# Performance work log

Hardware: AMD Instinct MI355X
Metric: run time of the kernel (lower is better)

## Reference

```python
import jax, jax.numpy as jnp
import numpy as np

N, E, F_IN, HID, HEADS, OUT, EDIM = 50000, 800000, 128, 64, 2, 40, 5
NEG_SLOPE = 0.2


def setup_inputs() -> dict:
    key = jax.random.key(0)
    ks = jax.random.split(key, 16)
    x = jax.random.normal(ks[0], (N, F_IN), jnp.float32)
    # build edge_index with src != dst so PyG's remove_self_loops is a no-op
    dst = jax.random.randint(ks[1], (E,), 0, N, dtype=jnp.int32)
    off = jax.random.randint(ks[2], (E,), 1, N, dtype=jnp.int32)
    src = (dst + off) % N
    edge_index = jnp.stack([src, dst], axis=0)
    edge_attr = jax.random.normal(ks[3], (E, EDIM), jnp.float32)
    s = 0.1
    params = dict(
        W1=jax.random.normal(ks[4], (F_IN, HEADS * HID), jnp.float32) * s,
        att_src1=jax.random.normal(ks[5], (HEADS, HID), jnp.float32) * s,
        att_dst1=jax.random.normal(ks[6], (HEADS, HID), jnp.float32) * s,
        We1=jax.random.normal(ks[7], (EDIM, HEADS * HID), jnp.float32) * s,
        att_e1=jax.random.normal(ks[8], (HEADS, HID), jnp.float32) * s,
        b1=jnp.zeros((HEADS * HID,), jnp.float32),
        W2=jax.random.normal(ks[9], (HEADS * HID, OUT), jnp.float32) * s,
        att_src2=jax.random.normal(ks[10], (1, OUT), jnp.float32) * s,
        att_dst2=jax.random.normal(ks[11], (1, OUT), jnp.float32) * s,
        We2=jax.random.normal(ks[12], (EDIM, OUT), jnp.float32) * s,
        att_e2=jax.random.normal(ks[13], (1, OUT), jnp.float32) * s,
        b2=jnp.zeros((OUT,), jnp.float32),
    )
    return dict(x=x, edge_index=edge_index, edge_attr=edge_attr, **params)


def _add_self_loops(src, dst, eattr, n):
    # PyG add_self_loops with fill_value='mean': per-dst-node mean of incoming edge_attr
    cnt = jax.ops.segment_sum(jnp.ones_like(dst, jnp.float32), dst, num_segments=n)
    loop_attr = jax.ops.segment_sum(eattr, dst, num_segments=n) / jnp.maximum(cnt, 1.0)[:, None]
    ar = jnp.arange(n, dtype=src.dtype)
    return (jnp.concatenate([src, ar]), jnp.concatenate([dst, ar]),
            jnp.concatenate([eattr, loop_attr], axis=0))


def _gat_conv(x, src, dst, eattr, W, a_src, a_dst, We, a_e, b):
    n = x.shape[0]
    H, C = a_src.shape
    xh = (x @ W).reshape(n, H, C)                      # [N,H,C]
    al_src = jnp.einsum('nhc,hc->nh', xh, a_src)[src]  # [Etot,H]
    al_dst = jnp.einsum('nhc,hc->nh', xh, a_dst)[dst]
    eh = (eattr @ We).reshape(-1, H, C)                # [Etot,H,C]
    al_e = jnp.einsum('ehc,hc->eh', eh, a_e)
    alpha = jax.nn.leaky_relu(al_src + al_dst + al_e, negative_slope=NEG_SLOPE)
    amax = jax.ops.segment_max(alpha, dst, num_segments=n)  # segment-wise softmax over dst
    ex = jnp.exp(alpha - amax[dst])
    denom = jax.ops.segment_sum(ex, dst, num_segments=n)
    alpha = ex / (denom[dst] + 1e-16)
    out = jax.ops.segment_sum(xh[src] * alpha[:, :, None], dst, num_segments=n)
    return out.reshape(n, H * C) + b


def reference(x, edge_index, edge_attr, W1, att_src1, att_dst1, We1, att_e1, b1,
              W2, att_src2, att_dst2, We2, att_e2, b2):
    src, dst = edge_index[0], edge_index[1]
    s2, d2, ea2 = _add_self_loops(src, dst, edge_attr, x.shape[0])
    h = jax.nn.elu(_gat_conv(x, s2, d2, ea2, W1, att_src1, att_dst1, We1, att_e1, b1))
    logits = _gat_conv(h, s2, d2, ea2, W2, att_src2, att_dst2, We2, att_e2, b2)
    return jax.nn.log_softmax(logits, axis=1)
```

## Files before the change

### kernel.cpp

```cpp
#include <hip/hip_runtime.h>
#include <hip/hip_fp16.h>
#include <math.h>

#define N_NODES 50000
#define N_EDGES 800000
#define F_IN    128
#define HID     64
#define HEADS   2
#define C1      128
#define OUT_C   40
#define EDIM    5
#define NEG_SLOPE 0.2f
#define CAPN    64
#define NPB1    16
#define NPB2    8
#define SCAN_B  256
#define SCAN_NB ((N_NODES + SCAN_B - 1) / SCAN_B)

typedef __bf16 bf16x8 __attribute__((ext_vector_type(8)));
typedef float  f32x4v __attribute__((ext_vector_type(4)));

constexpr size_t pad64(size_t n){ return (n + 63) / 64 * 64; }
constexpr size_t O_CNT      = 0;
constexpr size_t O_ZERO_END = O_CNT      + pad64(N_NODES);
constexpr size_t O_RANK     = O_ZERO_END;
constexpr size_t O_ROWPTR   = O_RANK     + pad64(N_EDGES);
constexpr size_t O_STMP     = O_ROWPTR   + pad64(N_NODES+1);
constexpr size_t O_BSUM     = O_STMP     + pad64(N_NODES);
constexpr size_t O_BOFF     = O_BSUM     + pad64(SCAN_NB);
constexpr size_t O_EREC     = O_BOFF     + pad64(SCAN_NB);
constexpr size_t O_WEATT    = O_EREC     + pad64((size_t)N_EDGES*2);
constexpr size_t O_XHB      = O_WEATT    + 64;
constexpr size_t O_AS1      = O_XHB      + pad64((size_t)N_NODES*C1/2);
constexpr size_t O_AD1      = O_AS1      + pad64((size_t)N_NODES*2);
constexpr size_t O_H1B      = O_AD1      + pad64((size_t)N_NODES*2);
constexpr size_t O_XH2B     = O_H1B      + pad64((size_t)N_NODES*C1/2);
constexpr size_t O_AS2      = O_XH2B     + pad64((size_t)N_NODES*OUT_C/2);
constexpr size_t O_AD2      = O_AS2      + pad64(N_NODES);

__device__ __forceinline__ float lrelu(float v){ return v >= 0.f ? v : NEG_SLOPE*v; }
__device__ __forceinline__ float bfl(unsigned u){ return __uint_as_float(u << 16); }
__device__ __forceinline__ float bfh(unsigned u){ return __uint_as_float(u & 0xFFFF0000u); }
__device__ __forceinline__ unsigned short f2bf(float f){
  unsigned u = __float_as_uint(f);
  return (unsigned short)((u + 0x7FFFu + ((u >> 16) & 1u)) >> 16);
}
__device__ __forceinline__ unsigned f2h(float f){
  return (unsigned)__half_as_ushort(__float2half(f));
}
__device__ __forceinline__ float h2f(unsigned u){
  return __half2float(__ushort_as_half((unsigned short)(u & 0xFFFFu)));
}

__global__ void k_zero(int* __restrict__ p, int n){
  int i = blockIdx.x*blockDim.x + threadIdx.x;
  if (i < n) p[i] = 0;
}

__global__ void k_count(const int* __restrict__ dst, int* __restrict__ cnt,
                        int* __restrict__ rank){
  int e = blockIdx.x*blockDim.x + threadIdx.x;
  if (e >= N_EDGES) return;
  rank[e] = atomicAdd(&cnt[dst[e]], 1);
}

__global__ void __launch_bounds__(SCAN_B) k_scan1(const int* __restrict__ cnt,
                                                  int* __restrict__ stmp,
                                                  int* __restrict__ bsum){
  int blk = blockIdx.x, t = threadIdx.x;
  int i = blk*SCAN_B + t;
  int v = (i < N_NODES) ? cnt[i] : 0;
  int lane = t & 63, w = t >> 6;
  int x = v;
  #pragma unroll
  for (int off = 1; off < 64; off <<= 1){
    int y = __shfl_up(x, off);
    if (lane >= off) x += y;
  }
  __shared__ int wsum[SCAN_B/64];
  if (lane == 63) wsum[w] = x;
  __syncthreads();
  int add = 0;
  for (int k = 0; k < w; k++) add += wsum[k];
  x += add;
  if (i < N_NODES) stmp[i] = x;
  if (t == SCAN_B-1) bsum[blk] = x;
}

__global__ void __launch_bounds__(SCAN_B) k_scan2(const int* __restrict__ bsum,
                                                  int* __restrict__ boff,
                                                  const float* __restrict__ We1,
                                                  const float* __restrict__ ae1,
                                                  const float* __restrict__ We2,
                                                  const float* __restrict__ ae2,
                                                  float* __restrict__ weatt){
  int t = threadIdx.x;
  int v = (t < SCAN_NB) ? bsum[t] : 0;
  int lane = t & 63, w = t >> 6;
  int x = v;
  #pragma unroll
  for (int off = 1; off < 64; off <<= 1){
    int y = __shfl_up(x, off);
    if (lane >= off) x += y;
  }
  __shared__ int wsum[SCAN_B/64];
  if (lane == 63) wsum[w] = x;
  __syncthreads();
  int add = 0;
  for (int k = 0; k < w; k++) add += wsum[k];
  x += add;
  if (t < SCAN_NB) boff[t] = x - v;
  if (t < 10){
    int k = t >> 1, h = t & 1;
    float s = 0.f;
    for (int c = 0; c < HID; c++) s += We1[k*C1 + h*HID + c] * ae1[h*HID + c];
    weatt[k*2 + h] = s;
  } else if (t < 15){
    int k = t - 10;
    float s = 0.f;
    for (int c = 0; c < OUT_C; c++) s += We2[k*OUT_C + c] * ae2[c];
    weatt[10 + k] = s;
  }
}

__global__ void __launch_bounds__(SCAN_B) k_scan3(const int* __restrict__ stmp,
                                                  const int* __restrict__ boff,
                                                  int* __restrict__ rowptr){
  int blk = blockIdx.x, t = threadIdx.x;
  int i = blk*SCAN_B + t;
  if (i < N_NODES) rowptr[i+1] = stmp[i] + boff[blk];
  if (i == 0) rowptr[0] = 0;
}

__global__ void k_scatter(const int* __restrict__ src, const int* __restrict__ dst,
                          const int* __restrict__ rank,
                          const float* __restrict__ eattr, const int* __restrict__ rowptr,
                          const float* __restrict__ weatt,
                          uint2* __restrict__ erec){
  int e = blockIdx.x*blockDim.x + threadIdx.x;
  if (e >= N_EDGES) return;
  int d = dst[e];
  int pos = rowptr[d] + rank[e];
  float a[EDIM];
  #pragma unroll
  for (int k = 0; k < EDIM; k++) a[k] = eattr[e*EDIM + k];
  float l0 = 0.f, l1 = 0.f, l2 = 0.f;
  #pragma unroll
  for (int k = 0; k < EDIM; k++){
    l0 += a[k]*weatt[k*2 + 0];
    l1 += a[k]*weatt[k*2 + 1];
    l2 += a[k]*weatt[10 + k];
  }
  unsigned w0 = (unsigned)src[e] | (f2h(l2) << 16);
  unsigned w1 = f2h(l0) | (f2h(l1) << 16);
  erec[pos] = make_uint2(w0, w1);
}

__global__ void __launch_bounds__(256) k_gemm1(const float* __restrict__ x,
                                               const float* __restrict__ W,
                                               const float* __restrict__ a_src,
                                               const float* __restrict__ a_dst,
                                               unsigned short* __restrict__ xhb,
                                               float* __restrict__ as_o,
                                               float* __restrict__ ad_o){
  __shared__ __align__(16) unsigned char smem[128*136*2];
  __bf16 (*wt)[136] = (__bf16(*)[136])smem;
  float  (*eps)[132] = (float(*)[132])smem;
  int tid = threadIdx.x;
  int wv = tid >> 6, L = tid & 63;
  int g = L >> 4, c16 = L & 15;
  int r0 = blockIdx.x * 64;

  for (int i = tid; i < F_IN*C1; i += 256){
    int k = i >> 7, c = i & 127;
    wt[c][k] = (__bf16)W[i];
  }
  __syncthreads();

  f32x4v acc[8];
  #pragma unroll
  for (int ct = 0; ct < 8; ct++) acc[ct] = (f32x4v){0.f, 0.f, 0.f, 0.f};

  int arow = r0 + wv*16 + c16;
  bool aok = arow < N_NODES;
  const float* xrow = &x[(size_t)arow*F_IN];
  #pragma unroll
  for (int ks = 0; ks < 4; ks++){
    int k0 = ks*32 + g*8;
    bf16x8 a;
    if (aok){
      float4 v0 = *(const float4*)&xrow[k0];
      float4 v1 = *(const float4*)&xrow[k0 + 4];
      a[0]=(__bf16)v0.x; a[1]=(__bf16)v0.y; a[2]=(__bf16)v0.z; a[3]=(__bf16)v0.w;
      a[4]=(__bf16)v1.x; a[5]=(__bf16)v1.y; a[6]=(__bf16)v1.z; a[7]=(__bf16)v1.w;
    } else {
      a = (bf16x8)(__bf16)0.f;
    }
    #pragma unroll
    for (int ct = 0; ct < 8; ct++){
      bf16x8 b = *(const bf16x8*)&wt[ct*16 + c16][k0];
      acc[ct] = __builtin_amdgcn_mfma_f32_16x16x32_bf16(a, b, acc[ct], 0, 0, 0);
    }
  }
  __syncthreads();

  #pragma unroll
  for (int ct = 0; ct < 8; ct++){
    #pragma unroll
    for (int r = 0; r < 4; r++)
      eps[wv*16 + g*4 + r][ct*16 + c16] = acc[ct][r];
  }
  __syncthreads();

  int row = tid >> 2, cb = tid & 3;
  int grow = r0 + row;
  float vals[32];
  #pragma unroll
  for (int j = 0; j < 32; j++) vals[j] = eps[row][cb*32 + j];
  if (grow < N_NODES){
    unsigned pk[16];
    #pragma unroll
    for (int j = 0; j < 16; j++)
      pk[j] = (unsigned)f2bf(vals[2*j]) | ((unsigned)f2bf(vals[2*j+1]) << 16);
    uint4* d4 = (uint4*)&xhb[(size_t)grow*C1 + cb*32];
    d4[0] = make_uint4(pk[0],pk[1],pk[2],pk[3]);
    d4[1] = make_uint4(pk[4],pk[5],pk[6],pk[7]);
    d4[2] = make_uint4(pk[8],pk[9],pk[10],pk[11]);
    d4[3] = make_uint4(pk[12],pk[13],pk[14],pk[15]);
  }
  float s = 0.f, d = 0.f;
  #pragma unroll
  for (int j = 0; j < 32; j++){
    s += vals[j]*a_src[cb*32 + j];
    d += vals[j]*a_dst[cb*32 + j];
  }
  s += __shfl_xor(s, 1);
  d += __shfl_xor(d, 1);
  if ((cb & 1) == 0 && grow < N_NODES){
    int h = cb >> 1;
    as_o[grow*2 + h] = s;
    ad_o[grow*2 + h] = d;
  }
}

__global__ void __launch_bounds__(256) k_agg1(const unsigned short* __restrict__ xhb,
    const int* __restrict__ rowptr, const uint2* __restrict__ erec,
    const float* __restrict__ as1, const float* __restrict__ ad1,
    const float* __restrict__ b1, unsigned short* __restrict__ h1b){
  __shared__ float2 eC[NPB1][CAPN+1];
  __shared__ int    sC[NPB1][CAPN+1];
  int t = threadIdx.x;
  int g = t >> 4, l = t & 15;
  int n = blockIdx.x*NPB1 + g;
  if (n >= N_NODES) return;
  int beg = rowptr[n], end = rowptr[n+1];
  int deg = end - beg;
  float2 adn = *(const float2*)&ad1[n*2];
  bool cached = (deg <= CAPN);

  float s0 = 0.f, s1 = 0.f, la0 = 0.f, la1 = 0.f;
  for (int i = l; i < deg; i += 16){
    uint2 r = erec[(size_t)beg + i];
    int s = r.x & 0xFFFFu;
    float al0 = h2f(r.y), al1 = h2f(r.y >> 16);
    float2 a = *(const float2*)&as1[s*2];
    float e0 = expf(lrelu(a.x + adn.x + al0));
    float e1 = expf(lrelu(a.y + adn.y + al1));
    if (cached){ sC[g][i] = s * C1; eC[g][i] = make_float2(e0, e1); }
    s0 += e0; s1 += e1; la0 += al0; la1 += al1;
  }
  #pragma unroll
  for (int off = 1; off < 16; off <<= 1){
    s0 += __shfl_xor(s0, off); s1 += __shfl_xor(s1, off);
    la0 += __shfl_xor(la0, off); la1 += __shfl_xor(la1, off);
  }
  float inv = 1.f / fmaxf((float)deg, 1.f);
  float2 asn = *(const float2*)&as1[n*2];
  float sl0 = lrelu(asn.x + adn.x + la0*inv);
  float sl1 = lrelu(asn.y + adn.y + la1*inv);
  float es0 = expf(sl0), es1 = expf(sl1);
  float S0 = s0 + es0 + 1e-16f;
  float S1 = s1 + es1 + 1e-16f;

  int head = l >> 3;
  float acc[8];
  #pragma unroll
  for (int j = 0; j < 8; j++) acc[j] = 0.f;
  if (cached){
    for (int k = 0; k < deg; k++){
      float2 e2 = eC[g][k];
      float e = head ? e2.y : e2.x;
      uint4 r = *(const uint4*)&xhb[sC[g][k] + l*8];
      acc[0] += e*bfl(r.x); acc[1] += e*bfh(r.x);
      acc[2] += e*bfl(r.y); acc[3] += e*bfh(r.y);
      acc[4] += e*bfl(r.z); acc[5] += e*bfh(r.z);
      acc[6] += e*bfl(r.w); acc[7] += e*bfh(r.w);
    }
  } else {
    for (int k = 0; k < deg; k++){
      uint2 rr = erec[(size_t)beg + k];
      int s = rr.x & 0xFFFFu;
      float2 a = *(const float2*)&as1[s*2];
      float e = head ? expf(lrelu(a.y + adn.y + h2f(rr.y >> 16)))
                     : expf(lrelu(a.x + adn.x + h2f(rr.y)));
      uint4 r = *(const uint4*)&xhb[(size_t)s*C1 + l*8];
      acc[0] += e*bfl(r.x); acc[1] += e*bfh(r.x);
      acc[2] += e*bfl(r.y); acc[3] += e*bfh(r.y);
      acc[4] += e*bfl(r.z); acc[5] += e*bfh(r.z);
      acc[6] += e*bfl(r.w); acc[7] += e*bfh(r.w);
    }
  }
  float es = head ? es1 : es0;
  float den = head ? S1 : S0;
  uint4 r = *(const uint4*)&xhb[(size_t)n*C1 + l*8];
  float xs8[8];
  xs8[0]=bfl(r.x); xs8[1]=bfh(r.x); xs8[2]=bfl(r.y); xs8[3]=bfh(r.y);
  xs8[4]=bfl(r.z); xs8[5]=bfh(r.z); xs8[6]=bfl(r.w); xs8[7]=bfh(r.w);
  unsigned pk[4];
  #pragma unroll
  for (int p = 0; p < 4; p++){
    float v0 = (acc[2*p]   + es*xs8[2*p])   / den + b1[l*8 + 2*p];
    float v1 = (acc[2*p+1] + es*xs8[2*p+1]) / den + b1[l*8 + 2*p+1];
    v0 = v0 > 0.f ? v0 : expm1f(v0);
    v1 = v1 > 0.f ? v1 : expm1f(v1);
    pk[p] = (unsigned)f2bf(v0) | ((unsigned)f2bf(v1) << 16);
  }
  *(uint4*)&h1b[(size_t)n*C1 + l*8] = make_uint4(pk[0], pk[1], pk[2], pk[3]);
}

__global__ void __launch_bounds__(256) k_gemm2(const unsigned short* __restrict__ h1b,
    const float* __restrict__ W2, const float* __restrict__ a_src2,
    const float* __restrict__ a_dst2,
    unsigned short* __restrict__ xh2b, float* __restrict__ as_o, float* __restrict__ ad_o){
  __shared__ __align__(16) unsigned char smem[64*52*4];
  __bf16 (*wt)[136] = (__bf16(*)[136])smem;
  float  (*eps)[52] = (float(*)[52])smem;
  int tid = threadIdx.x;
  int wv = tid >> 6, L = tid & 63;
  int g = L >> 4, c16 = L & 15;
  int r0 = blockIdx.x * 64;

  for (int i = tid; i < 48*F_IN; i += 256){
    int c = i >> 7, k = i & 127;
    wt[c][k] = (c < OUT_C) ? (__bf16)W2[k*OUT_C + c] : (__bf16)0.f;
  }
  __syncthreads();

  f32x4v acc[3];
  #pragma unroll
  for (int ct = 0; ct < 3; ct++) acc[ct] = (f32x4v){0.f, 0.f, 0.f, 0.f};

  int arow = r0 + wv*16 + c16;
  bool aok = arow < N_NODES;
  const unsigned short* hrow = &h1b[(size_t)arow*C1];
  #pragma unroll
  for (int ks = 0; ks < 4; ks++){
    int k0 = ks*32 + g*8;
    bf16x8 a;
    if (aok) a = *(const bf16x8*)&hrow[k0];
    else     a = (bf16x8)(__bf16)0.f;
    #pragma unroll
    for (int ct = 0; ct < 3; ct++){
      bf16x8 b = *(const bf16x8*)&wt[ct*16 + c16][k0];
      acc[ct] = __builtin_amdgcn_mfma_f32_16x16x32_bf16(a, b, acc[ct], 0, 0, 0);
    }
  }
  __syncthreads();

  #pragma unroll
  for (int ct = 0; ct < 3; ct++){
    #pragma unroll
    for (int r = 0; r < 4; r++)
      eps[wv*16 + g*4 + r][ct*16 + c16] = acc[ct][r];
  }
  __syncthreads();

  int row = tid >> 2, cb = tid & 3;
  int grow = r0 + row;
  int base = cb*12;
  float vals[12];
  #pragma unroll
  for (int j = 0; j < 12; j++) vals[j] = eps[row][base + j];
  int npair = (cb < 3) ? 6 : 2;
  if (grow < N_NODES){
    unsigned* dp = (unsigned*)&xh2b[(size_t)grow*OUT_C + base];
    for (int jj = 0; jj < npair; jj++)
      dp[jj] = (unsigned)f2bf(vals[2*jj]) | ((unsigned)f2bf(vals[2*jj+1]) << 16);
  }
  float s = 0.f, d = 0.f;
  #pragma unroll
  for (int j = 0; j < 12; j++){
    int col = base + j;
    if (col < OUT_C){
      s += vals[j]*a_src2[col];
      d += vals[j]*a_dst2[col];
    }
  }
  s += __shfl_xor(s, 1); s += __shfl_xor(s, 2);
  d += __shfl_xor(d, 1); d += __shfl_xor(d, 2);
  if (cb == 0 && grow < N_NODES){
    as_o[grow] = s;
    ad_o[grow] = d;
  }
}

__global__ void __launch_bounds__(256) k_agg2(const unsigned short* __restrict__ xh2b,
    const int* __restrict__ rowptr, const uint2* __restrict__ erec,
    const float* __restrict__ as2, const float* __restrict__ ad2,
    const float* __restrict__ b2, float* __restrict__ out){
  __shared__ float eC[NPB2][CAPN+1];
  __shared__ int   sC[NPB2][CAPN+1];
  int t = threadIdx.x;
  int g = t >> 5, l = t & 31;
  int n = blockIdx.x*NPB2 + g;
  if (n >= N_NODES) return;
  int beg = rowptr[n], end = rowptr[n+1];
  int deg = end - beg;
  float adv = ad2[n];
  bool cached = (deg <= CAPN);

  float ss = 0.f, la = 0.f;
  for (int i = l; i < deg; i += 32){
    uint2 r = erec[(size_t)beg + i];
    int s = r.x & 0xFFFFu;
    float al2 = h2f(r.x >> 16);
    float e = expf(lrelu(as2[s] + adv + al2));
    if (cached){ sC[g][i] = s * OUT_C; eC[g][i] = e; }
    ss += e; la += al2;
  }
  #pragma unroll
  for (int off = 1; off < 32; off <<= 1){
    ss += __shfl_xor(ss, off);
    la += __shfl_xor(la, off);
  }
  float inv = 1.f / fmaxf((float)deg, 1.f);
  float sl = lrelu(as2[n] + adv + la*inv);
  float es = expf(sl);
  float S = ss + es + 1e-16f;

  float a0 = 0.f, a1 = 0.f;
  if (l < 20){
    if (cached){
      for (int k = 0; k < deg; k++){
        float e = eC[g][k];
        unsigned u = *(const unsigned*)&xh2b[sC[g][k] + l*2];
        a0 += e*bfl(u); a1 += e*bfh(u);
      }
    } else {
      for (int k = 0; k < deg; k++){
        uint2 rr = erec[(size_t)beg + k];
        int s = rr.x & 0xFFFFu;
        float e = expf(lrelu(as2[s] + adv + h2f(rr.x >> 16)));
        unsigned u = *(const unsigned*)&xh2b[(size_t)s*OUT_C + l*2];
        a0 += e*bfl(u); a1 += e*bfh(u);
      }
    }
  }
  float o0 = -INFINITY, o1 = -INFINITY;
  if (l < 20){
    unsigned u = *(const unsigned*)&xh2b[(size_t)n*OUT_C + l*2];
    o0 = (a0 + es*bfl(u)) / S + b2[l*2 + 0];
    o1 = (a1 + es*bfh(u)) / S + b2[l*2 + 1];
  }
  float mm = fmaxf(o0, o1);
  #pragma unroll
  for (int off = 1; off < 32; off <<= 1) mm = fmaxf(mm, __shfl_xor(mm, off));
  float e = (l < 20) ? (expf(o0 - mm) + expf(o1 - mm)) : 0.f;
  #pragma unroll
  for (int off = 1; off < 32; off <<= 1) e += __shfl_xor(e, off);
  if (l < 20){
    float lse = logf(e);
    out[(size_t)n*OUT_C + l*2 + 0] = o0 - mm - lse;
    out[(size_t)n*OUT_C + l*2 + 1] = o1 - mm - lse;
  }
}

extern "C" void kernel_launch(void* const* d_in, const int* in_sizes, int n_in,
                              void* d_out, int out_size, void* d_ws, size_t ws_size,
                              hipStream_t stream){
  const float* x        = (const float*)d_in[0];
  const int*   ei       = (const int*)  d_in[1];
  const float* eattr    = (const float*)d_in[2];
  const float* W1       = (const float*)d_in[3];
  const float* att_src1 = (const float*)d_in[4];
  const float* att_dst1 = (const float*)d_in[5];
  const float* We1      = (const float*)d_in[6];
  const float* att_e1   = (const float*)d_in[7];
  const float* b1       = (const float*)d_in[8];
  const float* W2       = (const float*)d_in[9];
  const float* att_src2 = (const float*)d_in[10];
  const float* att_dst2 = (const float*)d_in[11];
  const float* We2      = (const float*)d_in[12];
  const float* att_e2   = (const float*)d_in[13];
  const float* b2       = (const float*)d_in[14];
  const int* src = ei;
  const int* dst = ei + N_EDGES;

  float* wsf    = (float*)d_ws;
  int*   cnt     = (int*)(wsf + O_CNT);
  int*   rank    = (int*)(wsf + O_RANK);
  int*   rowptr  = (int*)(wsf + O_ROWPTR);
  int*   stmp    = (int*)(wsf + O_STMP);
  int*   bsum    = (int*)(wsf + O_BSUM);
  int*   boff    = (int*)(wsf + O_BOFF);
  uint2* erec    = (uint2*)(wsf + O_EREC);
  float* weatt   = wsf + O_WEATT;
  unsigned short* xhb  = (unsigned short*)(wsf + O_XHB);
  float* as1     = wsf + O_AS1;
  float* ad1     = wsf + O_AD1;
  unsigned short* h1b  = (unsigned short*)(wsf + O_H1B);
  unsigned short* xh2b = (unsigned short*)(wsf + O_XH2B);
  float* as2     = wsf + O_AS2;
  float* ad2     = wsf + O_AD2;
  float* out     = (float*)d_out;

  const int NZ = (int)O_ZERO_END;
  const int EB = (N_EDGES + 255) / 256;

  k_zero   <<<(NZ + 255)/256, 256, 0, stream>>>(cnt, NZ);
  k_count  <<<EB, 256, 0, stream>>>(dst, cnt, rank);
  k_scan1  <<<SCAN_NB, SCAN_B, 0, stream>>>(cnt, stmp, bsum);
  k_scan2  <<<1, SCAN_B, 0, stream>>>(bsum, boff, We1, att_e1, We2, att_e2, weatt);
  k_scan3  <<<SCAN_NB, SCAN_B, 0, stream>>>(stmp, boff, rowptr);
  k_scatter<<<EB, 256, 0, stream>>>(src, dst, rank, eattr, rowptr, weatt, erec);

  k_gemm1  <<<(N_NODES + 63)/64, 256, 0, stream>>>(x, W1, att_src1, att_dst1, xhb, as1, ad1);
  k_agg1   <<<(N_NODES + NPB1 - 1)/NPB1, 256, 0, stream>>>(xhb, rowptr, erec, as1, ad1, b1, h1b);

  k_gemm2  <<<(N_NODES + 63)/64, 256, 0, stream>>>(h1b, W2, att_src2, att_dst2, xh2b, as2, ad2);
  k_agg2   <<<(N_NODES + NPB2 - 1)/NPB2, 256, 0, stream>>>(xh2b, rowptr, erec, as2, ad2, b2, out);
}
```

Measured before the change: 167.2 us.

## Fuse edge counting with first GEMM and drop explicit rowptr materialization

```diff
diff --git a/kernel.cpp b/kernel.cpp
--- a/kernel.cpp
+++ b/kernel.cpp
@@ -16,6 +16,8 @@
 #define NPB2    8
 #define SCAN_B  256
 #define SCAN_NB ((N_NODES + SCAN_B - 1) / SCAN_B)
+#define G1B     ((N_NODES + 63) / 64)
+#define EB      ((N_EDGES + 255) / 256)
 
 typedef __bf16 bf16x8 __attribute__((ext_vector_type(8)));
 typedef float  f32x4v __attribute__((ext_vector_type(4)));
@@ -24,8 +26,7 @@
 constexpr size_t O_CNT      = 0;
 constexpr size_t O_ZERO_END = O_CNT      + pad64(N_NODES);
 constexpr size_t O_RANK     = O_ZERO_END;
-constexpr size_t O_ROWPTR   = O_RANK     + pad64(N_EDGES);
-constexpr size_t O_STMP     = O_ROWPTR   + pad64(N_NODES+1);
+constexpr size_t O_STMP     = O_RANK     + pad64(N_EDGES);
 constexpr size_t O_BSUM     = O_STMP     + pad64(N_NODES);
 constexpr size_t O_BOFF     = O_BSUM     + pad64(SCAN_NB);
 constexpr size_t O_EREC     = O_BOFF     + pad64(SCAN_NB);
@@ -51,125 +52,51 @@
 __device__ __forceinline__ float h2f(unsigned u){
   return __half2float(__ushort_as_half((unsigned short)(u & 0xFFFFu)));
 }
-
-__global__ void k_zero(int* __restrict__ p, int n){
+__device__ __forceinline__ int rowptr_at(const int* __restrict__ stmp,
+                                         const int* __restrict__ boff, int d){
+  return d ? (stmp[d-1] + boff[(d-1) >> 8]) : 0;
+}
+
+__global__ void k_init(int* __restrict__ p, int n,
+                       const float* __restrict__ We1, const float* __restrict__ ae1,
+                       const float* __restrict__ We2, const float* __restrict__ ae2,
+                       float* __restrict__ weatt){
   int i = blockIdx.x*blockDim.x + threadIdx.x;
   if (i < n) p[i] = 0;
-}
-
-__global__ void k_count(const int* __restrict__ dst, int* __restrict__ cnt,
-                        int* __restrict__ rank){
-  int e = blockIdx.x*blockDim.x + threadIdx.x;
-  if (e >= N_EDGES) return;
-  rank[e] = atomicAdd(&cnt[dst[e]], 1);
-}
-
-__global__ void __launch_bounds__(SCAN_B) k_scan1(const int* __restrict__ cnt,
-                                                  int* __restrict__ stmp,
-                                                  int* __restrict__ bsum){
-  int blk = blockIdx.x, t = threadIdx.x;
-  int i = blk*SCAN_B + t;
-  int v = (i < N_NODES) ? cnt[i] : 0;
-  int lane = t & 63, w = t >> 6;
-  int x = v;
-  #pragma unroll
-  for (int off = 1; off < 64; off <<= 1){
-    int y = __shfl_up(x, off);
-    if (lane >= off) x += y;
-  }
-  __shared__ int wsum[SCAN_B/64];
-  if (lane == 63) wsum[w] = x;
-  __syncthreads();
-  int add = 0;
-  for (int k = 0; k < w; k++) add += wsum[k];
-  x += add;
-  if (i < N_NODES) stmp[i] = x;
-  if (t == SCAN_B-1) bsum[blk] = x;
-}
-
-__global__ void __launch_bounds__(SCAN_B) k_scan2(const int* __restrict__ bsum,
-                                                  int* __restrict__ boff,
-                                                  const float* __restrict__ We1,
-                                                  const float* __restrict__ ae1,
-                                                  const float* __restrict__ We2,
-                                                  const float* __restrict__ ae2,
-                                                  float* __restrict__ weatt){
-  int t = threadIdx.x;
-  int v = (t < SCAN_NB) ? bsum[t] : 0;
-  int lane = t & 63, w = t >> 6;
-  int x = v;
-  #pragma unroll
-  for (int off = 1; off < 64; off <<= 1){
-    int y = __shfl_up(x, off);
-    if (lane >= off) x += y;
-  }
-  __shared__ int wsum[SCAN_B/64];
-  if (lane == 63) wsum[w] = x;
-  __syncthreads();
-  int add = 0;
-  for (int k = 0; k < w; k++) add += wsum[k];
-  x += add;
-  if (t < SCAN_NB) boff[t] = x - v;
-  if (t < 10){
-    int k = t >> 1, h = t & 1;
-    float s = 0.f;
-    for (int c = 0; c < HID; c++) s += We1[k*C1 + h*HID + c] * ae1[h*HID + c];
-    weatt[k*2 + h] = s;
-  } else if (t < 15){
-    int k = t - 10;
-    float s = 0.f;
-    for (int c = 0; c < OUT_C; c++) s += We2[k*OUT_C + c] * ae2[c];
-    weatt[10 + k] = s;
-  }
-}
-
-__global__ void __launch_bounds__(SCAN_B) k_scan3(const int* __restrict__ stmp,
-                                                  const int* __restrict__ boff,
-                                                  int* __restrict__ rowptr){
-  int blk = blockIdx.x, t = threadIdx.x;
-  int i = blk*SCAN_B + t;
-  if (i < N_NODES) rowptr[i+1] = stmp[i] + boff[blk];
-  if (i == 0) rowptr[0] = 0;
-}
-
-__global__ void k_scatter(const int* __restrict__ src, const int* __restrict__ dst,
-                          const int* __restrict__ rank,
-                          const float* __restrict__ eattr, const int* __restrict__ rowptr,
-                          const float* __restrict__ weatt,
-                          uint2* __restrict__ erec){
-  int e = blockIdx.x*blockDim.x + threadIdx.x;
-  if (e >= N_EDGES) return;
-  int d = dst[e];
-  int pos = rowptr[d] + rank[e];
-  float a[EDIM];
-  #pragma unroll
-  for (int k = 0; k < EDIM; k++) a[k] = eattr[e*EDIM + k];
-  float l0 = 0.f, l1 = 0.f, l2 = 0.f;
-  #pragma unroll
-  for (int k = 0; k < EDIM; k++){
-    l0 += a[k]*weatt[k*2 + 0];
-    l1 += a[k]*weatt[k*2 + 1];
-    l2 += a[k]*weatt[10 + k];
-  }
-  unsigned w0 = (unsigned)src[e] | (f2h(l2) << 16);
-  unsigned w1 = f2h(l0) | (f2h(l1) << 16);
-  erec[pos] = make_uint2(w0, w1);
-}
-
-__global__ void __launch_bounds__(256) k_gemm1(const float* __restrict__ x,
-                                               const float* __restrict__ W,
-                                               const float* __restrict__ a_src,
-                                               const float* __restrict__ a_dst,
-                                               unsigned short* __restrict__ xhb,
-                                               float* __restrict__ as_o,
-                                               float* __restrict__ ad_o){
+  if (blockIdx.x == 0){
+    int t = threadIdx.x;
+    if (t < 10){
+      int k = t >> 1, h = t & 1;
+      float s = 0.f;
+      for (int c = 0; c < HID; c++) s += We1[k*C1 + h*HID + c] * ae1[h*HID + c];
+      weatt[k*2 + h] = s;
+    } else if (t < 15){
+      int k = t - 10;
+      float s = 0.f;
+      for (int c = 0; c < OUT_C; c++) s += We2[k*OUT_C + c] * ae2[c];
+      weatt[10 + k] = s;
+    }
+  }
+}
+
+__global__ void __launch_bounds__(256) k_count_gemm1(
+    const int* __restrict__ dst, int* __restrict__ cnt, int* __restrict__ rank,
+    const float* __restrict__ x, const float* __restrict__ W,
+    const float* __restrict__ a_src, const float* __restrict__ a_dst,
+    unsigned short* __restrict__ xhb, float* __restrict__ as_o, float* __restrict__ ad_o){
   __shared__ __align__(16) unsigned char smem[128*136*2];
+  int bid = blockIdx.x;
+  if (bid < EB){
+    int e = bid*256 + threadIdx.x;
+    if (e < N_EDGES) rank[e] = atomicAdd(&cnt[dst[e]], 1);
+    return;
+  }
   __bf16 (*wt)[136] = (__bf16(*)[136])smem;
   float  (*eps)[132] = (float(*)[132])smem;
   int tid = threadIdx.x;
   int wv = tid >> 6, L = tid & 63;
   int g = L >> 4, c16 = L & 15;
-  int r0 = blockIdx.x * 64;
+  int r0 = (bid - EB) * 64;
 
   for (int i = tid; i < F_IN*C1; i += 256){
     int k = i >> 7, c = i & 127;
@@ -243,8 +170,77 @@
   }
 }
 
+__global__ void __launch_bounds__(SCAN_B) k_scan1(const int* __restrict__ cnt,
+                                                  int* __restrict__ stmp,
+                                                  int* __restrict__ bsum){
+  int blk = blockIdx.x, t = threadIdx.x;
+  int i = blk*SCAN_B + t;
+  int v = (i < N_NODES) ? cnt[i] : 0;
+  int lane = t & 63, w = t >> 6;
+  int x = v;
+  #pragma unroll
+  for (int off = 1; off < 64; off <<= 1){
+    int y = __shfl_up(x, off);
+    if (lane >= off) x += y;
+  }
+  __shared__ int wsum[SCAN_B/64];
+  if (lane == 63) wsum[w] = x;
+  __syncthreads();
+  int add = 0;
+  for (int k = 0; k < w; k++) add += wsum[k];
+  x += add;
+  if (i < N_NODES) stmp[i] = x;
+  if (t == SCAN_B-1) bsum[blk] = x;
+}
+
+__global__ void __launch_bounds__(SCAN_B) k_scan2(const int* __restrict__ bsum,
+                                                  int* __restrict__ boff){
+  int t = threadIdx.x;
+  int v = (t < SCAN_NB) ? bsum[t] : 0;
+  int lane = t & 63, w = t >> 6;
+  int x = v;
+  #pragma unroll
+  for (int off = 1; off < 64; off <<= 1){
+    int y = __shfl_up(x, off);
+    if (lane >= off) x += y;
+  }
+  __shared__ int wsum[SCAN_B/64];
+  if (lane == 63) wsum[w] = x;
+  __syncthreads();
+  int add = 0;
+  for (int k = 0; k < w; k++) add += wsum[k];
+  x += add;
+  if (t < SCAN_NB) boff[t] = x - v;
+}
+
+__global__ void k_scatter(const int* __restrict__ src, const int* __restrict__ dst,
+                          const int* __restrict__ rank,
+                          const float* __restrict__ eattr,
+                          const int* __restrict__ stmp, const int* __restrict__ boff,
+                          const float* __restrict__ weatt,
+                          uint2* __restrict__ erec){
+  int e = blockIdx.x*blockDim.x + threadIdx.x;
+  if (e >= N_EDGES) return;
+  int d = dst[e];
+  int pos = rowptr_at(stmp, boff, d) + rank[e];
+  float a[EDIM];
+  #pragma unroll
+  for (int k = 0; k < EDIM; k++) a[k] = eattr[e*EDIM + k];
+  float l0 = 0.f, l1 = 0.f, l2 = 0.f;
+  #pragma unroll
+  for (int k = 0; k < EDIM; k++){
+    l0 += a[k]*weatt[k*2 + 0];
+    l1 += a[k]*weatt[k*2 + 1];
+    l2 += a[k]*weatt[10 + k];
+  }
+  unsigned w0 = (unsigned)src[e] | (f2h(l2) << 16);
+  unsigned w1 = f2h(l0) | (f2h(l1) << 16);
+  erec[pos] = make_uint2(w0, w1);
+}
+
 __global__ void __launch_bounds__(256) k_agg1(const unsigned short* __restrict__ xhb,
-    const int* __restrict__ rowptr, const uint2* __restrict__ erec,
+    const int* __restrict__ stmp, const int* __restrict__ boff,
+    const uint2* __restrict__ erec,
     const float* __restrict__ as1, const float* __restrict__ ad1,
     const float* __restrict__ b1, unsigned short* __restrict__ h1b){
   __shared__ float2 eC[NPB1][CAPN+1];
@@ -253,7 +249,8 @@
   int g = t >> 4, l = t & 15;
   int n = blockIdx.x*NPB1 + g;
   if (n >= N_NODES) return;
-  int beg = rowptr[n], end = rowptr[n+1];
+  int beg = rowptr_at(stmp, boff, n);
+  int end = stmp[n] + boff[n >> 8];
   int deg = end - beg;
   float2 adn = *(const float2*)&ad1[n*2];
   bool cached = (deg <= CAPN);
@@ -405,7 +402,8 @@
 }
 
 __global__ void __launch_bounds__(256) k_agg2(const unsigned short* __restrict__ xh2b,
-    const int* __restrict__ rowptr, const uint2* __restrict__ erec,
+    const int* __restrict__ stmp, const int* __restrict__ boff,
+    const uint2* __restrict__ erec,
     const float* __restrict__ as2, const float* __restrict__ ad2,
     const float* __restrict__ b2, float* __restrict__ out){
   __shared__ float eC[NPB2][CAPN+1];
@@ -414,7 +412,8 @@
   int g = t >> 5, l = t & 31;
   int n = blockIdx.x*NPB2 + g;
   if (n >= N_NODES) return;
-  int beg = rowptr[n], end = rowptr[n+1];
+  int beg = rowptr_at(stmp, boff, n);
+  int end = stmp[n] + boff[n >> 8];
   int deg = end - beg;
   float adv = ad2[n];
   bool cached = (deg <= CAPN);
@@ -499,7 +498,6 @@
   float* wsf    = (float*)d_ws;
   int*   cnt     = (int*)(wsf + O_CNT);
   int*   rank    = (int*)(wsf + O_RANK);
-  int*   rowptr  = (int*)(wsf + O_ROWPTR);
   int*   stmp    = (int*)(wsf + O_STMP);
   int*   bsum    = (int*)(wsf + O_BSUM);
   int*   boff    = (int*)(wsf + O_BOFF);
@@ -515,18 +513,17 @@
   float* out     = (float*)d_out;
 
   const int NZ = (int)O_ZERO_END;
-  const int EB = (N_EDGES + 255) / 256;
-
-  k_zero   <<<(NZ + 255)/256, 256, 0, stream>>>(cnt, NZ);
-  k_count  <<<EB, 256, 0, stream>>>(dst, cnt, rank);
+
+  k_init   <<<(NZ + 255)/256, 256, 0, stream>>>(cnt, NZ, We1, att_e1, We2, att_e2, weatt);
+  k_count_gemm1<<<EB + G1B, 256, 0, stream>>>(dst, cnt, rank,
+                                              x, W1, att_src1, att_dst1, xhb, as1, ad1);
   k_scan1  <<<SCAN_NB, SCAN_B, 0, stream>>>(cnt, stmp, bsum);
-  k_scan2  <<<1, SCAN_B, 0, stream>>>(bsum, boff, We1, att_e1, We2, att_e2, weatt);
-  k_scan3  <<<SCAN_NB, SCAN_B, 0, stream>>>(stmp, boff, rowptr);
-  k_scatter<<<EB, 256, 0, stream>>>(src, dst, rank, eattr, rowptr, weatt, erec);
-
-  k_gemm1  <<<(N_NODES + 63)/64, 256, 0, stream>>>(x, W1, att_src1, att_dst1, xhb, as1, ad1);
-  k_agg1   <<<(N_NODES + NPB1 - 1)/NPB1, 256, 0, stream>>>(xhb, rowptr, erec, as1, ad1, b1, h1b);
-
+  k_scan2  <<<1, SCAN_B, 0, stream>>>(bsum, boff);
+  k_scatter<<<EB, 256, 0, stream>>>(src, dst, rank, eattr, stmp, boff, weatt, erec);
+
+  k_agg1   <<<(N_NODES + NPB1 - 1)/NPB1, 256, 0, stream>>>(xhb, stmp, boff, erec,
+                                                           as1, ad1, b1, h1b);
   k_gemm2  <<<(N_NODES + 63)/64, 256, 0, stream>>>(h1b, W2, att_src2, att_dst2, xh2b, as2, ad2);
-  k_agg2   <<<(N_NODES + NPB2 - 1)/NPB2, 256, 0, stream>>>(xh2b, rowptr, erec, as2, ad2, b2, out);
-}
+  k_agg2   <<<(N_NODES + NPB2 - 1)/NPB2, 256, 0, stream>>>(xh2b, stmp, boff, erec,
+                                                           as2, ad2, b2, out);
+}
```

After: 161.5 us. 3.4% less time.
